# Optimization experiments

Hardware: AMD Instinct MI355X
Metric: run time of the kernel (lower is better)

## Reference

```python
import jax, jax.numpy as jnp
import numpy as np
import math

BLOCK_SIZE = 64
GATE_HIDDEN = 128


def _rmsnorm(x, w, eps=1e-6):
    v = jnp.mean(jnp.square(x), axis=-1, keepdims=True)
    return x * jax.lax.rsqrt(v + eps) * w


def _rotate_half(x):
    x1, x2 = jnp.split(x, 2, axis=-1)
    return jnp.concatenate([-x2, x1], axis=-1)


def _rope(x, cos, sin):
    # x: [B, S, H, D]; cos/sin: [B, S, D] -> unsqueeze head dim (unsqueeze_dim=2)
    c = cos[:, :, None, :]
    s = sin[:, :, None, :]
    return x * c + _rotate_half(x) * s


def setup_inputs() -> dict:
    key = jax.random.key(0)
    ks = jax.random.split(key, 10)
    B, S, Hk, D = 4, 65536, 8, 128
    Hq, g, Dg = 32, 4, GATE_HIDDEN
    nb = S // BLOCK_SIZE
    xav_q = math.sqrt(6.0 / (D + Dg))
    xav_k = math.sqrt(6.0 / (2 * D + Dg))
    return {
        "k": jax.random.normal(ks[0], (B, S, Hk, D), jnp.float32),
        "q": jax.random.normal(ks[1], (B, 1, Hq, D), jnp.float32),
        "Wq": jax.random.uniform(ks[2], (Hk, g, D, Dg), jnp.float32, -xav_q, xav_q),
        "Wk": jax.random.uniform(ks[3], (Hk, 2 * D, Dg), jnp.float32, -xav_k, xav_k),
        "qnorm_w": jnp.ones((Dg,), jnp.float32),
        "knorm_w": jnp.ones((Dg,), jnp.float32),
        "cos_q": jax.random.uniform(ks[4], (B, 1, Dg), jnp.float32, -1.0, 1.0),
        "sin_q": jax.random.uniform(ks[5], (B, 1, Dg), jnp.float32, -1.0, 1.0),
        "cos_k": jax.random.uniform(ks[6], (B, nb, Dg), jnp.float32, -1.0, 1.0),
        "sin_k": jax.random.uniform(ks[7], (B, nb, Dg), jnp.float32, -1.0, 1.0),
        "attention_mask": jnp.ones((B, Hk, nb), jnp.bool_),
        "block_budget": 128,
    }


def reference(k, q, Wq, Wk, qnorm_w, knorm_w, cos_q, sin_q, cos_k, sin_k,
              attention_mask, block_budget):
    B, S, Hk, D = k.shape
    nb = S // BLOCK_SIZE
    g = q.shape[2] // Hk
    Dg = Wk.shape[-1]
    scale = 1.0 / math.sqrt(Dg)

    # --- K path: block pooling (avg + max) -> per-head linear -> RMSNorm -> RoPE
    kb = k.reshape(B, nb, BLOCK_SIZE, Hk, D)
    k_pooled = jnp.concatenate([kb.mean(axis=2), kb.max(axis=2)], axis=-1)  # [B,nb,Hk,2D]
    k_c = jnp.einsum('bshi,hio->bsho', k_pooled, Wk)                         # [B,nb,Hk,Dg]
    k_c = _rmsnorm(k_c, knorm_w)
    k_c = _rope(k_c, cos_k, sin_k)

    # --- Q path (Qproj): grouped per-k-head projection -> RMSNorm -> RoPE
    qg = q.reshape(B, 1, Hk, g, D)
    qp = jnp.einsum('bskgi,kgio->bsko', qg, Wq)                              # [B,1,Hk,Dg]
    qp = _rmsnorm(qp, qnorm_w)
    qp = _rope(qp, cos_q, sin_q)
    qv = qp[:, 0]                                                            # [B,Hk,Dg]

    # --- gate scores + softmax
    attn = jnp.einsum('bhd,bshd->bhs', qv, k_c) * scale                      # [B,Hk,nb]
    attn = jnp.where(attention_mask, attn, jnp.float32(-1e20))
    attn = jax.nn.softmax(attn, axis=-1)

    # --- token_budget sparse block mask: topk + scatter
    _, topk_idx = jax.lax.top_k(attn, block_budget)                          # [B,Hk,k]
    blk = jnp.arange(nb)
    mask = jnp.any(topk_idx[..., :, None] == blk[None, None, None, :], axis=-2)
    mask = mask & attention_mask
    mask = mask.at[:, :, -1].set(True)
    return mask
```

## Files before the change

### kernel.cpp

```cpp
#include <hip/hip_runtime.h>
#include <hip/hip_bf16.h>
#include <math.h>

#define NB   1024
#define HKH  8
#define DGD  128

typedef float f4 __attribute__((ext_vector_type(4)));

__global__ __launch_bounds__(256) void pool_kernel(const float* __restrict__ kin,
                                                   float* __restrict__ pooled) {
    int blkid = blockIdx.x;
    int t = threadIdx.x;
    const f4* src = (const f4*)kin + (size_t)blkid * 16384 + t;
    f4 v = __builtin_nontemporal_load(src);
    f4 s = v, m = v;
#pragma unroll 8
    for (int r = 1; r < 64; ++r) {
        f4 u = __builtin_nontemporal_load(src + (size_t)r * 256);
        s.x += u.x; s.y += u.y; s.z += u.z; s.w += u.w;
        m.x = fmaxf(m.x, u.x); m.y = fmaxf(m.y, u.y);
        m.z = fmaxf(m.z, u.z); m.w = fmaxf(m.w, u.w);
    }
    int h = t >> 5;
    int d = (t & 31) << 2;
    float* dst = pooled + ((size_t)blkid * HKH + h) * 256 + d;
    const float inv = 1.0f / 64.0f;
    f4 mean = { s.x * inv, s.y * inv, s.z * inv, s.w * inv };
    *(f4*)dst         = mean;
    *(f4*)(dst + 128) = m;
}

__global__ __launch_bounds__(512) void qproj_kernel(const float* __restrict__ q,
                                                    const float* __restrict__ Wq,
                                                    const float* __restrict__ qnw,
                                                    const float* __restrict__ cq,
                                                    const float* __restrict__ sq,
                                                    float* __restrict__ qv) {
    int b = blockIdx.x >> 3, h = blockIdx.x & 7;
    int t = threadIdx.x;
    int o = t & 127, seg = t >> 7;
    __shared__ float qs[512];
    __shared__ float part[4][128];
    __shared__ float red[2];
    __shared__ float ybuf[128];
    qs[t] = q[(size_t)b * 4096 + (size_t)h * 512 + t];
    __syncthreads();
    const float* wqp = Wq + (size_t)h * 512 * 128 + o;
    float acc = 0.0f;
    int g0 = seg * 128;
#pragma unroll 4
    for (int gi = g0; gi < g0 + 128; ++gi)
        acc = fmaf(qs[gi], wqp[(size_t)gi * 128], acc);
    part[seg][o] = acc;
    __syncthreads();
    if (t < 128) {
        float a = part[0][o] + part[1][o] + part[2][o] + part[3][o];
        ybuf[o] = a;
        float ss = a * a;
        for (int off = 32; off > 0; off >>= 1) ss += __shfl_xor(ss, off);
        if ((o & 63) == 0) red[o >> 6] = ss;
    }
    __syncthreads();
    if (t < 128) {
        float scale = rsqrtf((red[0] + red[1]) * (1.0f / 128.0f) + 1e-6f);
        float y  = ybuf[o] * scale * qnw[o];
        int op   = (o < 64) ? o + 64 : o - 64;
        float yp = ybuf[op] * scale * qnw[op];
        float rot = (o < 64) ? -yp : yp;
        qv[((size_t)b * HKH + h) * 128 + o] =
            fmaf(y, cq[b * 128 + o], rot * sq[b * 128 + o]);
    }
}

__global__ __launch_bounds__(256) void kscore_kernel(const float* __restrict__ pooled,
                                                     const float* __restrict__ Wk,
                                                     const float* __restrict__ knw,
                                                     const float* __restrict__ cosk,
                                                     const float* __restrict__ sink,
                                                     const float* __restrict__ qv,
                                                     float* __restrict__ scores) {
    __shared__ float As[64][64];
    __shared__ float Ws[64][128];
    int h  = blockIdx.y;
    int m0 = blockIdx.x * 64;
    int b  = m0 >> 10;
    int t  = threadIdx.x;
    int tc = t & 15, tr = t >> 4;
    int sw3 = tr & 3;

    float acc[4][8];
#pragma unroll
    for (int i = 0; i < 4; ++i)
#pragma unroll
        for (int j = 0; j < 8; ++j) acc[i][j] = 0.0f;

    for (int kk = 0; kk < 256; kk += 64) {
#pragma unroll
        for (int ii = 0; ii < 4; ++ii) {
            int idx = t + ii * 256;
            int lr = idx >> 4, f4i = idx & 15;
            f4 v = *(const f4*)(pooled + ((size_t)(m0 + lr) * HKH + h) * 256 + kk + f4i * 4);
            *(f4*)&As[lr][(f4i ^ (lr & 3)) << 2] = v;
        }
#pragma unroll
        for (int ii = 0; ii < 8; ++ii) {
            int idx = t + ii * 256;
            int kw = idx >> 5, f4i = idx & 31;
            f4 v = *(const f4*)(Wk + ((size_t)h * 256 + kk + kw) * 128 + f4i * 4);
            *(f4*)&Ws[kw][f4i * 4] = v;
        }
        __syncthreads();
#pragma unroll
        for (int k4 = 0; k4 < 16; ++k4) {
            f4 a4[4];
            int swc = ((k4 ^ sw3) << 2);
#pragma unroll
            for (int i = 0; i < 4; ++i) a4[i] = *(const f4*)&As[tr + 16 * i][swc];
            f4 wlo[4], whi[4];
#pragma unroll
            for (int dk = 0; dk < 4; ++dk) {
                wlo[dk] = *(const f4*)&Ws[k4 * 4 + dk][tc * 4];
                whi[dk] = *(const f4*)&Ws[k4 * 4 + dk][64 + tc * 4];
            }
#pragma unroll
            for (int dk = 0; dk < 4; ++dk) {
#pragma unroll
                for (int i = 0; i < 4; ++i) {
                    float a = (dk == 0) ? a4[i].x : (dk == 1) ? a4[i].y : (dk == 2) ? a4[i].z : a4[i].w;
                    acc[i][0] = fmaf(a, wlo[dk].x, acc[i][0]);
                    acc[i][1] = fmaf(a, wlo[dk].y, acc[i][1]);
                    acc[i][2] = fmaf(a, wlo[dk].z, acc[i][2]);
                    acc[i][3] = fmaf(a, wlo[dk].w, acc[i][3]);
                    acc[i][4] = fmaf(a, whi[dk].x, acc[i][4]);
                    acc[i][5] = fmaf(a, whi[dk].y, acc[i][5]);
                    acc[i][6] = fmaf(a, whi[dk].z, acc[i][6]);
                    acc[i][7] = fmaf(a, whi[dk].w, acc[i][7]);
                }
            }
        }
        __syncthreads();
    }

    float knlo[4], knhi[4], qlo[4], qhi[4];
    const float* qvp = qv + ((size_t)b * HKH + h) * 128;
#pragma unroll
    for (int j = 0; j < 4; ++j) {
        knlo[j] = knw[tc * 4 + j];      knhi[j] = knw[64 + tc * 4 + j];
        qlo[j]  = qvp[tc * 4 + j];      qhi[j]  = qvp[64 + tc * 4 + j];
    }
#pragma unroll
    for (int i = 0; i < 4; ++i) {
        int lr  = tr + 16 * i;
        int m   = m0 + lr;
        int blk = m & (NB - 1);
        float ss = 0.0f;
#pragma unroll
        for (int j = 0; j < 8; ++j) ss = fmaf(acc[i][j], acc[i][j], ss);
#pragma unroll
        for (int off = 1; off < 16; off <<= 1) ss += __shfl_xor(ss, off);
        float scale = rsqrtf(ss * (1.0f / 128.0f) + 1e-6f);
        const float* cb = cosk + ((size_t)b * NB + blk) * 128;
        const float* sb = sink + ((size_t)b * NB + blk) * 128;
        float part = 0.0f;
#pragma unroll
        for (int j = 0; j < 4; ++j) {
            int olo = tc * 4 + j, ohi = 64 + tc * 4 + j;
            float ylo = acc[i][j]     * scale * knlo[j];
            float yhi = acc[i][4 + j] * scale * knhi[j];
            float zlo = fmaf(ylo, cb[olo], -(yhi * sb[olo]));
            float zhi = fmaf(yhi, cb[ohi],  (ylo * sb[ohi]));
            part = fmaf(zlo, qlo[j], part);
            part = fmaf(zhi, qhi[j], part);
        }
#pragma unroll
        for (int off = 1; off < 16; off <<= 1) part += __shfl_xor(part, off);
        if (tc == 0)
            scores[((size_t)b * HKH + h) * NB + blk] = part * 0.08838834764831845f;
    }
}

__device__ inline bool read_mask(const void* amp, int mode, size_t idx) {
    if (mode == 1) return ((const int*)amp)[idx] != 0;
    if (mode == 2) return ((const unsigned int*)amp)[idx] != 0u;
    return ((const unsigned char*)amp)[idx] != 0;
}

__global__ __launch_bounds__(512) void topk_kernel(const float* __restrict__ scores,
                                                   const void* __restrict__ amraw,
                                                   const int* __restrict__ bbp,
                                                   int* __restrict__ out) {
    int b = blockIdx.x >> 3, h = blockIdx.x & 7;
    int t = threadIdx.x;
    __shared__ float sv[NB];
    __shared__ int mode_sh;

    if (t == 0) {
        const unsigned int* w = (const unsigned int*)amraw;
        bool allint = true, allflt = true;
        for (int i = 0; i < 64; ++i) {
            unsigned int x = w[i];
            if (x != 0u && x != 1u) allint = false;
            if (x != 0u && x != 0x3f800000u) allflt = false;
        }
        mode_sh = allint ? 1 : (allflt ? 2 : 0);
    }
    __syncthreads();
    int mode = mode_sh;
    size_t rowoff = ((size_t)b * HKH + h) * NB;
    const float* src = scores + rowoff;
    for (int s = t; s < NB; s += 512)
        sv[s] = read_mask(amraw, mode, rowoff + s) ? src[s] : -1e20f;
    __syncthreads();

    int bb = bbp[0];
    if (bb > NB) bb = NB;
    if (bb < 1)  bb = 1;

    int e0 = t, e1 = t + 512;
    float v0 = sv[e0], v1 = sv[e1];
    int r0 = 0, r1 = 0;
#pragma unroll 4
    for (int j4 = 0; j4 < 256; ++j4) {
        f4 w = *(const f4*)&sv[j4 * 4];
        int jb = j4 * 4;
        r0 += (w.x > v0) + (w.y > v0) + (w.z > v0) + (w.w > v0);
        r1 += (w.x > v1) + (w.y > v1) + (w.z > v1) + (w.w > v1);
        r0 += (w.x == v0 && jb + 0 < e0) + (w.y == v0 && jb + 1 < e0)
            + (w.z == v0 && jb + 2 < e0) + (w.w == v0 && jb + 3 < e0);
        r1 += (w.x == v1 && jb + 0 < e1) + (w.y == v1 && jb + 1 < e1)
            + (w.z == v1 && jb + 2 < e1) + (w.w == v1 && jb + 3 < e1);
    }
    int* dst = out + rowoff;
    bool am0 = read_mask(amraw, mode, rowoff + e0);
    bool am1 = read_mask(amraw, mode, rowoff + e1);
    dst[e0] = ((r0 < bb && am0)) ? 1 : 0;
    dst[e1] = ((r1 < bb && am1) || (e1 == NB - 1)) ? 1 : 0;
}

extern "C" void kernel_launch(void* const* d_in, const int* in_sizes, int n_in,
                              void* d_out, int out_size, void* d_ws, size_t ws_size,
                              hipStream_t stream) {
    (void)in_sizes; (void)n_in; (void)out_size; (void)ws_size;
    const float* k   = (const float*)d_in[0];
    const float* q   = (const float*)d_in[1];
    const float* Wq  = (const float*)d_in[2];
    const float* Wk  = (const float*)d_in[3];
    const float* qnw = (const float*)d_in[4];
    const float* knw = (const float*)d_in[5];
    const float* cq  = (const float*)d_in[6];
    const float* sq  = (const float*)d_in[7];
    const float* ck  = (const float*)d_in[8];
    const float* sk  = (const float*)d_in[9];
    const void*  am  = d_in[10];
    const int*   bb  = (const int*)d_in[11];
    int* out = (int*)d_out;

    float* pooled = (float*)d_ws;
    float* qv     = pooled + (size_t)4 * 1024 * 8 * 256;
    float* scores = qv + 4 * HKH * 128;

    pool_kernel<<<4096, 256, 0, stream>>>(k, pooled);
    qproj_kernel<<<32, 512, 0, stream>>>(q, Wq, qnw, cq, sq, qv);
    dim3 gb(64, 8);
    kscore_kernel<<<gb, 256, 0, stream>>>(pooled, Wk, knw, ck, sk, qv, scores);
    topk_kernel<<<32, 512, 0, stream>>>(scores, am, bb, out);
}
```

Before: 286.9 us.

## Fuse block pooling into projection-score kernel, dropping pooled workspace

Pooling of K blocks (mean and max) now happens inside the projection/score kernel. Each workgroup pools 16 blocks for one head into a transposed shared-memory tile, then runs the per-head projection, RMSNorm, RoPE and score dot product. This removes the separate pool kernel and the round trip of the pooled tensor through global memory. In exchange, each workgroup reads per-head 512-byte segments strided across rows, which may reduce DRAM access efficiency. The inner GEMM also has less register reuse per thread.

```diff
diff --git a/kernel.cpp b/kernel.cpp
--- a/kernel.cpp
+++ b/kernel.cpp
@@ -4,32 +4,8 @@
 
 #define NB   1024
 #define HKH  8
-#define DGD  128
 
 typedef float f4 __attribute__((ext_vector_type(4)));
-
-__global__ __launch_bounds__(256) void pool_kernel(const float* __restrict__ kin,
-                                                   float* __restrict__ pooled) {
-    int blkid = blockIdx.x;
-    int t = threadIdx.x;
-    const f4* src = (const f4*)kin + (size_t)blkid * 16384 + t;
-    f4 v = __builtin_nontemporal_load(src);
-    f4 s = v, m = v;
-#pragma unroll 8
-    for (int r = 1; r < 64; ++r) {
-        f4 u = __builtin_nontemporal_load(src + (size_t)r * 256);
-        s.x += u.x; s.y += u.y; s.z += u.z; s.w += u.w;
-        m.x = fmaxf(m.x, u.x); m.y = fmaxf(m.y, u.y);
-        m.z = fmaxf(m.z, u.z); m.w = fmaxf(m.w, u.w);
-    }
-    int h = t >> 5;
-    int d = (t & 31) << 2;
-    float* dst = pooled + ((size_t)blkid * HKH + h) * 256 + d;
-    const float inv = 1.0f / 64.0f;
-    f4 mean = { s.x * inv, s.y * inv, s.z * inv, s.w * inv };
-    *(f4*)dst         = mean;
-    *(f4*)(dst + 128) = m;
-}
 
 __global__ __launch_bounds__(512) void qproj_kernel(const float* __restrict__ q,
                                                     const float* __restrict__ Wq,
@@ -73,111 +49,103 @@
     }
 }
 
-__global__ __launch_bounds__(256) void kscore_kernel(const float* __restrict__ pooled,
-                                                     const float* __restrict__ Wk,
-                                                     const float* __restrict__ knw,
-                                                     const float* __restrict__ cosk,
-                                                     const float* __restrict__ sink,
-                                                     const float* __restrict__ qv,
-                                                     float* __restrict__ scores) {
-    __shared__ float As[64][64];
+__global__ __launch_bounds__(256) void fused_kernel(const float* __restrict__ kin,
+                                                    const float* __restrict__ Wk,
+                                                    const float* __restrict__ knw,
+                                                    const float* __restrict__ cosk,
+                                                    const float* __restrict__ sink,
+                                                    const float* __restrict__ qv,
+                                                    float* __restrict__ scores) {
+    __shared__ float At[256][17];
     __shared__ float Ws[64][128];
-    int h  = blockIdx.y;
-    int m0 = blockIdx.x * 64;
-    int b  = m0 >> 10;
-    int t  = threadIdx.x;
+    int wg   = blockIdx.x;
+    int tile = wg & 63;
+    int h    = (wg >> 6) & 7;
+    int b    = wg >> 9;
+    int t    = threadIdx.x;
+
+    {
+        int f4lane = t & 31;
+        int halfw  = t >> 5;
+        const float inv = 1.0f / 64.0f;
+#pragma unroll
+        for (int bi = 0; bi < 2; ++bi) {
+            int blk = halfw * 2 + bi;
+            size_t s0 = (size_t)b * 65536 + ((size_t)tile * 16 + blk) * 64;
+            const f4* src = (const f4*)(kin + s0 * 1024 + (size_t)h * 128) + f4lane;
+            f4 v = __builtin_nontemporal_load(src);
+            f4 s = v, m = v;
+#pragma unroll 8
+            for (int r = 1; r < 64; ++r) {
+                f4 u = __builtin_nontemporal_load(src + (size_t)r * 256);
+                s += u;
+                m.x = fmaxf(m.x, u.x); m.y = fmaxf(m.y, u.y);
+                m.z = fmaxf(m.z, u.z); m.w = fmaxf(m.w, u.w);
+            }
+            int k0 = f4lane * 4;
+            At[k0 + 0][blk] = s.x * inv; At[k0 + 1][blk] = s.y * inv;
+            At[k0 + 2][blk] = s.z * inv; At[k0 + 3][blk] = s.w * inv;
+            At[128 + k0 + 0][blk] = m.x; At[128 + k0 + 1][blk] = m.y;
+            At[128 + k0 + 2][blk] = m.z; At[128 + k0 + 3][blk] = m.w;
+        }
+    }
+
     int tc = t & 15, tr = t >> 4;
-    int sw3 = tr & 3;
-
-    float acc[4][8];
-#pragma unroll
-    for (int i = 0; i < 4; ++i)
-#pragma unroll
-        for (int j = 0; j < 8; ++j) acc[i][j] = 0.0f;
+    float acc[8];
+#pragma unroll
+    for (int j = 0; j < 8; ++j) acc[j] = 0.0f;
 
     for (int kk = 0; kk < 256; kk += 64) {
-#pragma unroll
-        for (int ii = 0; ii < 4; ++ii) {
-            int idx = t + ii * 256;
-            int lr = idx >> 4, f4i = idx & 15;
-            f4 v = *(const f4*)(pooled + ((size_t)(m0 + lr) * HKH + h) * 256 + kk + f4i * 4);
-            *(f4*)&As[lr][(f4i ^ (lr & 3)) << 2] = v;
-        }
+        __syncthreads();
 #pragma unroll
         for (int ii = 0; ii < 8; ++ii) {
             int idx = t + ii * 256;
-            int kw = idx >> 5, f4i = idx & 31;
-            f4 v = *(const f4*)(Wk + ((size_t)h * 256 + kk + kw) * 128 + f4i * 4);
-            *(f4*)&Ws[kw][f4i * 4] = v;
+            int kw = idx >> 5, c4 = idx & 31;
+            *(f4*)&Ws[kw][c4 * 4] =
+                *(const f4*)(Wk + ((size_t)h * 256 + kk + kw) * 128 + c4 * 4);
         }
         __syncthreads();
 #pragma unroll
-        for (int k4 = 0; k4 < 16; ++k4) {
-            f4 a4[4];
-            int swc = ((k4 ^ sw3) << 2);
-#pragma unroll
-            for (int i = 0; i < 4; ++i) a4[i] = *(const f4*)&As[tr + 16 * i][swc];
-            f4 wlo[4], whi[4];
-#pragma unroll
-            for (int dk = 0; dk < 4; ++dk) {
-                wlo[dk] = *(const f4*)&Ws[k4 * 4 + dk][tc * 4];
-                whi[dk] = *(const f4*)&Ws[k4 * 4 + dk][64 + tc * 4];
-            }
-#pragma unroll
-            for (int dk = 0; dk < 4; ++dk) {
-#pragma unroll
-                for (int i = 0; i < 4; ++i) {
-                    float a = (dk == 0) ? a4[i].x : (dk == 1) ? a4[i].y : (dk == 2) ? a4[i].z : a4[i].w;
-                    acc[i][0] = fmaf(a, wlo[dk].x, acc[i][0]);
-                    acc[i][1] = fmaf(a, wlo[dk].y, acc[i][1]);
-                    acc[i][2] = fmaf(a, wlo[dk].z, acc[i][2]);
-                    acc[i][3] = fmaf(a, wlo[dk].w, acc[i][3]);
-                    acc[i][4] = fmaf(a, whi[dk].x, acc[i][4]);
-                    acc[i][5] = fmaf(a, whi[dk].y, acc[i][5]);
-                    acc[i][6] = fmaf(a, whi[dk].z, acc[i][6]);
-                    acc[i][7] = fmaf(a, whi[dk].w, acc[i][7]);
-                }
-            }
-        }
-        __syncthreads();
-    }
-
-    float knlo[4], knhi[4], qlo[4], qhi[4];
+        for (int k = 0; k < 64; ++k) {
+            float a = At[kk + k][tr];
+            f4 wlo = *(const f4*)&Ws[k][tc * 4];
+            f4 whi = *(const f4*)&Ws[k][64 + tc * 4];
+            acc[0] = fmaf(a, wlo.x, acc[0]);
+            acc[1] = fmaf(a, wlo.y, acc[1]);
+            acc[2] = fmaf(a, wlo.z, acc[2]);
+            acc[3] = fmaf(a, wlo.w, acc[3]);
+            acc[4] = fmaf(a, whi.x, acc[4]);
+            acc[5] = fmaf(a, whi.y, acc[5]);
+            acc[6] = fmaf(a, whi.z, acc[6]);
+            acc[7] = fmaf(a, whi.w, acc[7]);
+        }
+    }
+
+    int blkg = tile * 16 + tr;
+    float ss = 0.0f;
+#pragma unroll
+    for (int j = 0; j < 8; ++j) ss = fmaf(acc[j], acc[j], ss);
+#pragma unroll
+    for (int off = 1; off < 16; off <<= 1) ss += __shfl_xor(ss, off);
+    float scale = rsqrtf(ss * (1.0f / 128.0f) + 1e-6f);
+    const float* cb  = cosk + ((size_t)b * NB + blkg) * 128;
+    const float* sb  = sink + ((size_t)b * NB + blkg) * 128;
     const float* qvp = qv + ((size_t)b * HKH + h) * 128;
+    float part = 0.0f;
 #pragma unroll
     for (int j = 0; j < 4; ++j) {
-        knlo[j] = knw[tc * 4 + j];      knhi[j] = knw[64 + tc * 4 + j];
-        qlo[j]  = qvp[tc * 4 + j];      qhi[j]  = qvp[64 + tc * 4 + j];
-    }
-#pragma unroll
-    for (int i = 0; i < 4; ++i) {
-        int lr  = tr + 16 * i;
-        int m   = m0 + lr;
-        int blk = m & (NB - 1);
-        float ss = 0.0f;
-#pragma unroll
-        for (int j = 0; j < 8; ++j) ss = fmaf(acc[i][j], acc[i][j], ss);
-#pragma unroll
-        for (int off = 1; off < 16; off <<= 1) ss += __shfl_xor(ss, off);
-        float scale = rsqrtf(ss * (1.0f / 128.0f) + 1e-6f);
-        const float* cb = cosk + ((size_t)b * NB + blk) * 128;
-        const float* sb = sink + ((size_t)b * NB + blk) * 128;
-        float part = 0.0f;
-#pragma unroll
-        for (int j = 0; j < 4; ++j) {
-            int olo = tc * 4 + j, ohi = 64 + tc * 4 + j;
-            float ylo = acc[i][j]     * scale * knlo[j];
-            float yhi = acc[i][4 + j] * scale * knhi[j];
-            float zlo = fmaf(ylo, cb[olo], -(yhi * sb[olo]));
-            float zhi = fmaf(yhi, cb[ohi],  (ylo * sb[ohi]));
-            part = fmaf(zlo, qlo[j], part);
-            part = fmaf(zhi, qhi[j], part);
-        }
-#pragma unroll
-        for (int off = 1; off < 16; off <<= 1) part += __shfl_xor(part, off);
-        if (tc == 0)
-            scores[((size_t)b * HKH + h) * NB + blk] = part * 0.08838834764831845f;
-    }
+        int olo = tc * 4 + j, ohi = 64 + olo;
+        float ylo = acc[j]     * scale * knw[olo];
+        float yhi = acc[4 + j] * scale * knw[ohi];
+        float zlo = fmaf(ylo, cb[olo], -(yhi * sb[olo]));
+        float zhi = fmaf(yhi, cb[ohi],  ylo * sb[ohi]);
+        part = fmaf(zlo, qvp[olo], part);
+        part = fmaf(zhi, qvp[ohi], part);
+    }
+#pragma unroll
+    for (int off = 1; off < 16; off <<= 1) part += __shfl_xor(part, off);
+    if (tc == 0)
+        scores[((size_t)b * HKH + h) * NB + blkg] = part * 0.08838834764831845f;
 }
 
 __device__ inline bool read_mask(const void* amp, int mode, size_t idx) {
@@ -256,13 +224,10 @@
     const int*   bb  = (const int*)d_in[11];
     int* out = (int*)d_out;
 
-    float* pooled = (float*)d_ws;
-    float* qv     = pooled + (size_t)4 * 1024 * 8 * 256;
+    float* qv     = (float*)d_ws;
     float* scores = qv + 4 * HKH * 128;
 
-    pool_kernel<<<4096, 256, 0, stream>>>(k, pooled);
     qproj_kernel<<<32, 512, 0, stream>>>(q, Wq, qnw, cq, sq, qv);
-    dim3 gb(64, 8);
-    kscore_kernel<<<gb, 256, 0, stream>>>(pooled, Wk, knw, ck, sk, qv, scores);
+    fused_kernel<<<2048, 256, 0, stream>>>(k, Wk, knw, ck, sk, qv, scores);
     topk_kernel<<<32, 512, 0, stream>>>(scores, am, bb, out);
 }
```

Measured after the change: 264.2 us. 7.9% less time.
